# Kernel tuning notes

Measured on AMD Instinct MI355X. Metric: run time of the kernel, lower is better.

The kernel has to match this reference:

```python
import jax, jax.numpy as jnp
import numpy as np

OUT_FEATURES = 4096
IN_FEATURES = 4096
NNZ = 838860
N_COLS = 8192


def setup_inputs() -> dict:
    key = jax.random.key(0)
    k_r, k_c, k_v, k_x = jax.random.split(key, 4)
    rows = jax.random.randint(k_r, (NNZ,), 0, OUT_FEATURES, dtype=jnp.int32)
    cols = jax.random.randint(k_c, (NNZ,), 0, IN_FEATURES, dtype=jnp.int32)
    vals = jax.random.normal(k_v, (NNZ,), dtype=jnp.float32)
    x = jax.random.normal(k_x, (IN_FEATURES, N_COLS), dtype=jnp.float32)
    return {"rows": rows, "cols": cols, "vals": vals, "x": x}


def reference(rows, cols, vals, x):
    # Sparse COO weight W[out, in]; duplicate (row, col) entries sum, matching
    # uncoalesced COO semantics of torch.sparse.mm.
    # Dense scatter + GEMM is the clean, efficient jax expression of the same math.
    W = jnp.zeros((OUT_FEATURES, IN_FEATURES), dtype=vals.dtype).at[rows, cols].add(vals)
    return W @ x  # [out_features, N]
```

## Files before the change

kernel.cpp:

```cpp
#include <hip/hip_runtime.h>

#define OUT_F 4096
#define IN_F  4096
#define NCOLS 8192

#define GM OUT_F
#define GK IN_F
#define GN NCOLS

typedef __attribute__((ext_vector_type(8))) short short8;
typedef __attribute__((ext_vector_type(4))) float f32x4;

__device__ inline unsigned short f2bf(float f) {
    union { float f; unsigned u; } c; c.f = f;
    unsigned u = c.u;
    u += 0x7fffu + ((u >> 16) & 1u);
    return (unsigned short)(u >> 16);
}

__device__ inline void gll16(const void* g, void* l) {
    __builtin_amdgcn_global_load_lds(
        (const __attribute__((address_space(1))) unsigned int*)g,
        (__attribute__((address_space(3))) unsigned int*)l, 16, 0, 0);
}

__global__ void scatter_dense(const int* __restrict__ rows, const int* __restrict__ cols,
                              const float* __restrict__ vals, float* __restrict__ W, int nnz) {
    int i = blockIdx.x * blockDim.x + threadIdx.x;
    if (i < nnz) atomicAdd(&W[(size_t)rows[i] * IN_F + cols[i]], vals[i]);
}

__global__ void convert_w(const float* __restrict__ Wf, unsigned short* __restrict__ Wb) {
    int i = blockIdx.x * blockDim.x + threadIdx.x;
    float4 v = ((const float4*)Wf)[i];
    ushort4 o;
    o.x = f2bf(v.x); o.y = f2bf(v.y); o.z = f2bf(v.z); o.w = f2bf(v.w);
    ((ushort4*)Wb)[i] = o;
}

__global__ __launch_bounds__(256) void transpose_x(const float* __restrict__ x,
                                                   unsigned short* __restrict__ xT) {
    __shared__ float tile[64][65];
    const int k0 = blockIdx.x * 64;
    const int n0 = blockIdx.y * 64;
    const int t = threadIdx.x;
    const int c4 = (t & 15) * 4;
    const int r0 = t >> 4;
    for (int p = 0; p < 4; ++p) {
        int r = r0 + p * 16;
        float4 v = *(const float4*)&x[(size_t)(k0 + r) * NCOLS + n0 + c4];
        tile[r][c4 + 0] = v.x; tile[r][c4 + 1] = v.y;
        tile[r][c4 + 2] = v.z; tile[r][c4 + 3] = v.w;
    }
    __syncthreads();
    const int n  = t >> 2;
    const int ks = (t & 3) * 16;
    unsigned w[8];
    for (int m = 0; m < 8; ++m) {
        unsigned short lo = f2bf(tile[ks + 2 * m + 0][n]);
        unsigned short hi = f2bf(tile[ks + 2 * m + 1][n]);
        w[m] = (unsigned)lo | ((unsigned)hi << 16);
    }
    uint4* dst = (uint4*)&xT[(size_t)(n0 + n) * GK + k0 + ks];
    dst[0] = make_uint4(w[0], w[1], w[2], w[3]);
    dst[1] = make_uint4(w[4], w[5], w[6], w[7]);
}

__global__ __launch_bounds__(256) void gemm_bt(const unsigned short* __restrict__ A,
                                               const unsigned short* __restrict__ BT,
                                               float* __restrict__ C) {
    __shared__ unsigned short As[128 * 64];
    __shared__ unsigned short Bs[128 * 64];

    const int tid  = threadIdx.x;
    const int wave = tid >> 6;
    const int lane = tid & 63;
    const int m0 = blockIdx.y * 128;
    const int n0 = blockIdx.x * 128;
    const int wm = (wave >> 1) * 64;
    const int wn = (wave & 1) * 64;
    const int lrow = lane >> 3;
    const int lk   = ((lane & 7) ^ (lrow & 7)) * 8;
    const int frow = lane & 15;
    const int jhi  = lane >> 4;

    f32x4 acc[4][4] = {};

    const unsigned short* aBase = A  + (size_t)(m0 + wave * 32 + lrow) * GK + lk;
    const unsigned short* bBase = BT + (size_t)(n0 + wave * 32 + lrow) * GK + lk;

    for (int kt = 0; kt < GK / 64; ++kt) {
        const int k0 = kt * 64;
        for (int j = 0; j < 4; ++j) {
            gll16(aBase + (size_t)j * 8 * GK + k0, &As[(wave * 4 + j) * 512]);
            gll16(bBase + (size_t)j * 8 * GK + k0, &Bs[(wave * 4 + j) * 512]);
        }
        __syncthreads();
        for (int s = 0; s < 2; ++s) {
            const int jblk = s * 4 + jhi;
            const int kswz = (jblk ^ (frow & 7)) * 8;
            short8 af[4], bq[4];
            for (int i = 0; i < 4; ++i)
                af[i] = *(const short8*)&As[(wm + i * 16 + frow) * 64 + kswz];
            for (int j = 0; j < 4; ++j)
                bq[j] = *(const short8*)&Bs[(wn + j * 16 + frow) * 64 + kswz];
            for (int i = 0; i < 4; ++i)
                for (int j = 0; j < 4; ++j)
                    acc[i][j] = __builtin_amdgcn_mfma_f32_16x16x32_bf16(
                        af[i], bq[j], acc[i][j], 0, 0, 0);
        }
        __syncthreads();
    }

    for (int i = 0; i < 4; ++i) {
        const int r0 = m0 + wm + i * 16 + (lane >> 4) * 4;
        for (int j = 0; j < 4; ++j) {
            const int cc = n0 + wn + j * 16 + frow;
            for (int r = 0; r < 4; ++r)
                C[(size_t)(r0 + r) * GN + cc] = acc[i][j][r];
        }
    }
}

#define WS_COUNTS  0
#define WS_OFFSETS 4097
#define WS_CURSOR  8194
#define WS_HEADER  12290

__global__ void hist_kernel(const int* __restrict__ rows, int* __restrict__ counts, int nnz) {
    int i = blockIdx.x * blockDim.x + threadIdx.x;
    if (i < nnz) atomicAdd(&counts[rows[i]], 1);
}

__global__ void scan_kernel(const int* __restrict__ counts, int* __restrict__ offsets) {
    __shared__ int lsum[256];
    int t = threadIdx.x;
    int base = t * 16;
    int local[16];
    int s = 0;
    for (int i = 0; i < 16; ++i) { local[i] = counts[base + i]; s += local[i]; }
    lsum[t] = s;
    __syncthreads();
    if (t == 0) {
        int acc = 0;
        for (int i = 0; i < 256; ++i) { int v = lsum[i]; lsum[i] = acc; acc += v; }
        offsets[OUT_F] = acc;
    }
    __syncthreads();
    int acc = lsum[t];
    for (int i = 0; i < 16; ++i) { offsets[base + i] = acc; acc += local[i]; }
}

__global__ void scatter_kernel(const int* __restrict__ rows, const int* __restrict__ cols,
                               const float* __restrict__ vals,
                               const int* __restrict__ offsets, int* __restrict__ cursor,
                               int* __restrict__ cols_s, float* __restrict__ vals_s, int nnz) {
    int i = blockIdx.x * blockDim.x + threadIdx.x;
    if (i < nnz) {
        int r = rows[i];
        int pos = offsets[r] + atomicAdd(&cursor[r], 1);
        cols_s[pos] = cols[i];
        vals_s[pos] = vals[i];
    }
}

__global__ __launch_bounds__(256) void spmm_kernel(const int* __restrict__ offsets,
                                                   const int* __restrict__ cols_s,
                                                   const float* __restrict__ vals_s,
                                                   const float* __restrict__ x,
                                                   float* __restrict__ out) {
    const int row  = blockIdx.x;
    const int col0 = blockIdx.y * 1024 + threadIdx.x * 4;
    const int k0 = offsets[row];
    const int k1 = offsets[row + 1];
    float4 acc = make_float4(0.f, 0.f, 0.f, 0.f);
    for (int k = k0; k < k1; ++k) {
        const int   c = cols_s[k];
        const float v = vals_s[k];
        const float4 xv = *reinterpret_cast<const float4*>(x + (size_t)c * NCOLS + col0);
        acc.x += v * xv.x;
        acc.y += v * xv.y;
        acc.z += v * xv.z;
        acc.w += v * xv.w;
    }
    *reinterpret_cast<float4*>(out + (size_t)row * NCOLS + col0) = acc;
}

extern "C" void kernel_launch(void* const* d_in, const int* in_sizes, int n_in,
                              void* d_out, int out_size, void* d_ws, size_t ws_size,
                              hipStream_t stream) {
    const int*   rows = (const int*)d_in[0];
    const int*   cols = (const int*)d_in[1];
    const float* vals = (const float*)d_in[2];
    const float* x    = (const float*)d_in[3];
    float*       out  = (float*)d_out;
    const int nnz = in_sizes[0];

    const size_t WF_BYTES = (size_t)GM * GK * 4;
    const size_t WB_BYTES = (size_t)GM * GK * 2;
    const size_t NEED = WF_BYTES + WB_BYTES;

    if (ws_size >= NEED) {
        float*          Wf = (float*)d_ws;
        unsigned short* Wb = (unsigned short*)((char*)d_ws + WF_BYTES);
        unsigned short* xT = (unsigned short*)d_ws;

        hipMemsetAsync(Wf, 0, WF_BYTES, stream);
        scatter_dense<<<(nnz + 255) / 256, 256, 0, stream>>>(rows, cols, vals, Wf, nnz);
        convert_w<<<(GM * GK / 4) / 256, 256, 0, stream>>>(Wf, Wb);
        dim3 tg(GK / 64, GN / 64);
        transpose_x<<<tg, 256, 0, stream>>>(x, xT);
        dim3 gg(GN / 128, GM / 128);
        gemm_bt<<<gg, 256, 0, stream>>>(Wb, xT, out);
    } else {
        int*   ws_i    = (int*)d_ws;
        int*   counts  = ws_i + WS_COUNTS;
        int*   offsets = ws_i + WS_OFFSETS;
        int*   cursor  = ws_i + WS_CURSOR;
        int*   cols_s  = ws_i + WS_HEADER;
        float* vals_s  = (float*)(ws_i + WS_HEADER + nnz);

        hipMemsetAsync(d_ws, 0, (size_t)WS_HEADER * sizeof(int), stream);
        const int nblk = (nnz + 255) / 256;
        hist_kernel<<<nblk, 256, 0, stream>>>(rows, counts, nnz);
        scan_kernel<<<1, 256, 0, stream>>>(counts, offsets);
        scatter_kernel<<<nblk, 256, 0, stream>>>(rows, cols, vals, offsets, cursor,
                                                 cols_s, vals_s, nnz);
        dim3 grid(OUT_F, NCOLS / 1024);
        spmm_kernel<<<grid, 256, 0, stream>>>(offsets, cols_s, vals_s, x, out);
    }
}
```

Before: 567.1 us.

## Replace 128x128 GEMM with pipelined 256x256 tile kernel using double-buffered LDS

Replaces the bf16 MFMA GEMM with a 512-thread kernel computing 256x256 output tiles. It double-buffers LDS in k-halves so async global-to-LDS loads overlap MFMA work, remaps workgroups with a swizzle for L2 locality, and raises MFMA priority with s_setprio. The aim is to hide the load latency and synchronisation stalls of the original single-buffered loop and to increase operand reuse per tile. The larger tile and 128 KB of LDS reduce occupancy and leave fewer blocks to fill the GPU.

```diff
diff --git a/kernel.cpp b/kernel.cpp
--- a/kernel.cpp
+++ b/kernel.cpp
@@ -66,58 +66,108 @@
     dst[1] = make_uint4(w[4], w[5], w[6], w[7]);
 }
 
-__global__ __launch_bounds__(256) void gemm_bt(const unsigned short* __restrict__ A,
-                                               const unsigned short* __restrict__ BT,
-                                               float* __restrict__ C) {
-    __shared__ unsigned short As[128 * 64];
-    __shared__ unsigned short Bs[128 * 64];
+__global__ __launch_bounds__(512, 2) void gemm256(const unsigned short* __restrict__ A,
+                                                  const unsigned short* __restrict__ BT,
+                                                  float* __restrict__ C) {
+    __shared__ unsigned short lds[8 * 8192];
 
     const int tid  = threadIdx.x;
     const int wave = tid >> 6;
     const int lane = tid & 63;
-    const int m0 = blockIdx.y * 128;
-    const int n0 = blockIdx.x * 128;
-    const int wm = (wave >> 1) * 64;
-    const int wn = (wave & 1) * 64;
-    const int lrow = lane >> 3;
-    const int lk   = ((lane & 7) ^ (lrow & 7)) * 8;
-    const int frow = lane & 15;
-    const int jhi  = lane >> 4;
-
-    f32x4 acc[4][4] = {};
-
-    const unsigned short* aBase = A  + (size_t)(m0 + wave * 32 + lrow) * GK + lk;
-    const unsigned short* bBase = BT + (size_t)(n0 + wave * 32 + lrow) * GK + lk;
-
-    for (int kt = 0; kt < GK / 64; ++kt) {
-        const int k0 = kt * 64;
-        for (int j = 0; j < 4; ++j) {
-            gll16(aBase + (size_t)j * 8 * GK + k0, &As[(wave * 4 + j) * 512]);
-            gll16(bBase + (size_t)j * 8 * GK + k0, &Bs[(wave * 4 + j) * 512]);
-        }
-        __syncthreads();
-        for (int s = 0; s < 2; ++s) {
-            const int jblk = s * 4 + jhi;
-            const int kswz = (jblk ^ (frow & 7)) * 8;
-            short8 af[4], bq[4];
-            for (int i = 0; i < 4; ++i)
-                af[i] = *(const short8*)&As[(wm + i * 16 + frow) * 64 + kswz];
-            for (int j = 0; j < 4; ++j)
-                bq[j] = *(const short8*)&Bs[(wn + j * 16 + frow) * 64 + kswz];
-            for (int i = 0; i < 4; ++i)
-                for (int j = 0; j < 4; ++j)
-                    acc[i][j] = __builtin_amdgcn_mfma_f32_16x16x32_bf16(
-                        af[i], bq[j], acc[i][j], 0, 0, 0);
-        }
-        __syncthreads();
-    }
-
-    for (int i = 0; i < 4; ++i) {
-        const int r0 = m0 + wm + i * 16 + (lane >> 4) * 4;
-        for (int j = 0; j < 4; ++j) {
-            const int cc = n0 + wn + j * 16 + frow;
+
+    const int wg  = blockIdx.y * 32 + blockIdx.x;
+    const int swz = (wg & 7) * 64 + (wg >> 3);
+    const int m0  = (swz >> 5) * 256;
+    const int n0  = (swz & 31) * 256;
+
+    const int wm = wave >> 2;
+    const int wn = wave & 3;
+
+    const int r0s  = tid >> 2;
+    const int swz0 = ((tid & 3) ^ (r0s & 3)) << 3;
+    const unsigned short* pA0 = A  + (size_t)(m0 + r0s) * GK + swz0;
+    const unsigned short* pA1 = pA0 + (size_t)128 * GK;
+    const unsigned short* pB0 = BT + (size_t)(n0 + r0s) * GK + swz0;
+    const unsigned short* pB1 = pB0 + (size_t)128 * GK;
+
+    const int frow  = lane & 15;
+    const int ajb   = ((lane >> 4) ^ (frow & 3)) << 3;
+    const int abase = ((wm << 7) + frow) * 32 + ajb;
+    const int bbase = ((wn << 6) + frow) * 32 + ajb;
+
+    f32x4 acc[8][4] = {};
+
+#define STAGE_A(bufc, khc, kt_) do {                                            \
+        const int koA_ = ((((kt_) & 63) << 6) + ((khc) << 5));                  \
+        gll16(pA0 + koA_, &lds[(((bufc) << 2) + (khc)) * 8192 + (wave << 9)]);  \
+        gll16(pA1 + koA_, &lds[(((bufc) << 2) + (khc)) * 8192 + 4096 + (wave << 9)]); \
+    } while (0)
+
+#define STAGE_B(bufc, khc, kt_) do {                                            \
+        const int koB_ = ((((kt_) & 63) << 6) + ((khc) << 5));                  \
+        gll16(pB0 + koB_, &lds[(((bufc) << 2) + 2 + (khc)) * 8192 + (wave << 9)]); \
+        gll16(pB1 + koB_, &lds[(((bufc) << 2) + 2 + (khc)) * 8192 + 4096 + (wave << 9)]); \
+    } while (0)
+
+    STAGE_A(0, 0, 0); STAGE_B(0, 0, 0);
+    STAGE_A(0, 1, 0); STAGE_B(0, 1, 0);
+    STAGE_A(1, 0, 1); STAGE_B(1, 0, 1);
+    asm volatile("s_waitcnt vmcnt(8)" ::: "memory");
+    __builtin_amdgcn_s_barrier();
+
+#define KHALF_BLOCK(bufc, khc, STAGE1, STAGE2) do {                             \
+        const unsigned short* Ar_ = &lds[(((bufc) << 2) + (khc)) * 8192];       \
+        const unsigned short* Br_ = &lds[(((bufc) << 2) + 2 + (khc)) * 8192];   \
+        short8 af[4], bf[4];                                                    \
+        _Pragma("unroll")                                                       \
+        for (int nj = 0; nj < 4; ++nj) bf[nj] = *(const short8*)&Br_[bbase + nj * 512]; \
+        _Pragma("unroll")                                                       \
+        for (int mi = 0; mi < 4; ++mi) af[mi] = *(const short8*)&Ar_[abase + mi * 512]; \
+        STAGE1;                                                                 \
+        __builtin_amdgcn_s_barrier();                                           \
+        __builtin_amdgcn_s_setprio(1);                                          \
+        _Pragma("unroll")                                                       \
+        for (int mi = 0; mi < 4; ++mi)                                          \
+            _Pragma("unroll")                                                   \
+            for (int nj = 0; nj < 4; ++nj)                                      \
+                acc[mi][nj] = __builtin_amdgcn_mfma_f32_16x16x32_bf16(          \
+                    af[mi], bf[nj], acc[mi][nj], 0, 0, 0);                      \
+        __builtin_amdgcn_s_setprio(0);                                          \
+        __builtin_amdgcn_s_barrier();                                           \
+        _Pragma("unroll")                                                       \
+        for (int mi = 0; mi < 4; ++mi) af[mi] = *(const short8*)&Ar_[abase + (4 + mi) * 512]; \
+        STAGE2;                                                                 \
+        __builtin_amdgcn_s_barrier();                                           \
+        __builtin_amdgcn_s_setprio(1);                                          \
+        _Pragma("unroll")                                                       \
+        for (int mi = 0; mi < 4; ++mi)                                          \
+            _Pragma("unroll")                                                   \
+            for (int nj = 0; nj < 4; ++nj)                                      \
+                acc[4 + mi][nj] = __builtin_amdgcn_mfma_f32_16x16x32_bf16(      \
+                    af[mi], bf[nj], acc[4 + mi][nj], 0, 0, 0);                  \
+        __builtin_amdgcn_s_setprio(0);                                          \
+        asm volatile("s_waitcnt vmcnt(8)" ::: "memory");                        \
+        __builtin_amdgcn_s_barrier();                                           \
+    } while (0)
+
+#pragma unroll 1
+    for (int it = 0; it < GK / 128; ++it) {
+        const int kt = it * 2;
+        KHALF_BLOCK(0, 0, STAGE_A(1, 1, kt + 1), STAGE_B(1, 1, kt + 1));
+        KHALF_BLOCK(0, 1, STAGE_A(0, 0, kt + 2), STAGE_B(0, 0, kt + 2));
+        KHALF_BLOCK(1, 0, STAGE_A(0, 1, kt + 2), STAGE_B(0, 1, kt + 2));
+        KHALF_BLOCK(1, 1, STAGE_A(1, 0, kt + 3), STAGE_B(1, 0, kt + 3));
+    }
+#undef KHALF_BLOCK
+#undef STAGE_A
+#undef STAGE_B
+
+    for (int mi = 0; mi < 8; ++mi) {
+        const int r0w = m0 + wm * 128 + mi * 16 + (lane >> 4) * 4;
+        for (int nj = 0; nj < 4; ++nj) {
+            const int cc = n0 + wn * 64 + nj * 16 + frow;
             for (int r = 0; r < 4; ++r)
-                C[(size_t)(r0 + r) * GN + cc] = acc[i][j][r];
+                C[(size_t)(r0w + r) * GN + cc] = acc[mi][nj][r];
         }
     }
 }
@@ -210,8 +260,8 @@
         convert_w<<<(GM * GK / 4) / 256, 256, 0, stream>>>(Wf, Wb);
         dim3 tg(GK / 64, GN / 64);
         transpose_x<<<tg, 256, 0, stream>>>(x, xT);
-        dim3 gg(GN / 128, GM / 128);
-        gemm_bt<<<gg, 256, 0, stream>>>(Wb, xT, out);
+        dim3 gg(GN / 256, GM / 256);
+        gemm256<<<gg, 512, 0, stream>>>(Wb, xT, out);
     } else {
         int*   ws_i    = (int*)d_ws;
         int*   counts  = ws_i + WS_COUNTS;
```

New measurement: 547.6 us. 1.04x faster.
